# Performance work log

Measured on AMD Instinct MI355X. Metric: run time of the kernel, lower is better.

## Reference

```python
import jax, jax.numpy as jnp
import numpy as np
import math

B, N, CZ, CH, H, NRBF = 1, 256, 128, 32, 4, 39
INF = 1e8
DMIN, DMAX = 3.25 / 10.0, 50.75 / 10.0
EPS = 1e-5


def _ln(x, g, b):
    mu = x.mean(-1, keepdims=True)
    var = ((x - mu) ** 2).mean(-1, keepdims=True)
    return (x - mu) / jnp.sqrt(var + EPS) * g + b


def _rbf(D):
    mu = jnp.linspace(DMIN, DMAX, NRBF)
    sigma = (DMAX - DMIN) / NRBF
    return jnp.exp(-(((D[..., None] - mu) / sigma) ** 2))  # [B,N,N,NRBF]


def _tri_attn(z, mask_bias, edge_bias, ln_g, ln_b, wq, wk, wv, wg, wo, starting):
    # z: [B,I,J,CZ]; mask_bias: [B,I,1,1,J]; edge_bias: [B,1,H,I,J]
    z = _ln(z, ln_g, ln_b)
    if not starting:
        z = jnp.swapaxes(z, -2, -3)
        mask_bias = jnp.swapaxes(mask_bias, -4, -1)
        edge_bias = jnp.swapaxes(edge_bias, -1, -2)
    sh = z.shape[:-1] + (H, CH)
    q = (z @ wq).reshape(sh)  # [B,I,Q,H,c]
    k = (z @ wk).reshape(sh)
    v = (z @ wv).reshape(sh)
    logits = jnp.einsum('biqhc,bikhc->bihqk', q, k) / math.sqrt(CH)
    logits = logits + mask_bias + edge_bias  # [B,I,H,Q,K]
    a = jax.nn.softmax(logits, axis=-1)
    o = jnp.einsum('bihqk,bikhc->biqhc', a, v)  # [B,I,Q,H,c]
    g = jax.nn.sigmoid((z @ wg).reshape(sh))
    o = (o * g).reshape(z.shape[:-1] + (H * CH,)) @ wo  # [B,I,Q,CZ]
    if not starting:
        o = jnp.swapaxes(o, -2, -3)
    return o


def setup_inputs() -> dict:
    key = jax.random.key(0)
    ks = iter(jax.random.split(key, 32))
    def w(shape, fan_in):
        return jax.random.normal(next(ks), shape, dtype=jnp.float32) / math.sqrt(fan_in)
    inp = {
        'edge_embed': jax.random.normal(next(ks), (B, N, N, CZ), dtype=jnp.float32),
        'coords': jax.random.normal(next(ks), (B, N, 3), dtype=jnp.float32),
        'edge_mask': jnp.ones((B, N, N), dtype=jnp.float32),
        'emb_rbf_w1': w((NRBF, CH), NRBF),
        'emb_rbf_ln_g': jnp.ones((CH,), jnp.float32),
        'emb_rbf_ln_b': jnp.zeros((CH,), jnp.float32),
        'emb_rbf_w2': w((CH, H), CH),
        'ln3_g': jnp.ones((CZ,), jnp.float32),
        'ln3_b': jnp.zeros((CZ,), jnp.float32),
        'emb_third_w': w((CZ, H), CZ),
    }
    for p in ('s', 'e'):
        inp[p + '_ln_g'] = jnp.ones((CZ,), jnp.float32)
        inp[p + '_ln_b'] = jnp.zeros((CZ,), jnp.float32)
        inp[p + '_wq'] = w((CZ, H * CH), CZ)
        inp[p + '_wk'] = w((CZ, H * CH), CZ)
        inp[p + '_wv'] = w((CZ, H * CH), CZ)
        inp[p + '_wg'] = w((CZ, H * CH), CZ)
        inp[p + '_wo'] = w((H * CH, CZ), H * CH)
    return inp


def reference(edge_embed, coords, edge_mask,
              emb_rbf_w1, emb_rbf_ln_g, emb_rbf_ln_b, emb_rbf_w2,
              ln3_g, ln3_b, emb_third_w,
              s_ln_g, s_ln_b, s_wq, s_wk, s_wv, s_wg, s_wo,
              e_ln_g, e_ln_b, e_wq, e_wk, e_wv, e_wg, e_wo):
    # pairwise distances [B,N,N]
    diff = coords[:, :, None, :] - coords[:, None, :, :]
    dist = jnp.sqrt(jnp.sum(diff * diff, axis=-1) + 1e-12)
    h = _rbf(dist) @ emb_rbf_w1
    h = _ln(h, emb_rbf_ln_g, emb_rbf_ln_b)
    dist_bias = h @ emb_rbf_w2  # [B,N,N,H]
    mask_bias = (edge_mask[..., :, None, None, :] - 1.0) * INF  # [B,N,1,1,N]
    third = _ln(edge_embed, ln3_g, ln3_b) @ emb_third_w  # [B,N,N,H]
    edge_bias = (dist_bias + third)[:, None]  # [B,1,N,N,H]
    edge_bias = jnp.moveaxis(edge_bias, -1, -3)  # permute_final_dims (2,0,1) -> [B,1,H,N,N]
    z = edge_embed
    z = z + _tri_attn(z, mask_bias, edge_bias, s_ln_g, s_ln_b, s_wq, s_wk, s_wv, s_wg, s_wo, True)
    z = z + _tri_attn(z, mask_bias, edge_bias, e_ln_g, e_ln_b, e_wq, e_wk, e_wv, e_wg, e_wo, False)
    return z
```

## Files before the change

kernel.cpp:

```cpp
#include <hip/hip_runtime.h>

typedef unsigned short u16;
typedef unsigned int u32;
typedef __attribute__((ext_vector_type(4))) short short4v;
typedef __attribute__((ext_vector_type(8))) short short8;
typedef __attribute__((ext_vector_type(4))) float f32x4;
typedef __attribute__((ext_vector_type(4))) u32 u32x4;

__device__ __forceinline__ float bf2f(u16 u){ u32 x = ((u32)u)<<16; float f; __builtin_memcpy(&f,&x,4); return f; }
__device__ __forceinline__ u16 f2bf(float f){ u32 u; __builtin_memcpy(&u,&f,4); u32 r = (u + 0x7fffu + ((u>>16)&1u))>>16; return (u16)r; }

__device__ __forceinline__ float wsum64(float v){
  #pragma unroll
  for (int m=32;m>=1;m>>=1) v += __shfl_xor(v,m,64);
  return v;
}
__device__ __forceinline__ float wsum32(float v){
  #pragma unroll
  for (int m=16;m>=1;m>>=1) v += __shfl_xor(v,m,64);
  return v;
}

struct WPtrs { const float* s[10]; u16* d[10]; };

__global__ __launch_bounds__(256) void kconv_all(WPtrs wp){
  int mid = blockIdx.x>>6;
  int t = (blockIdx.x&63)*256 + threadIdx.x;
  int n = t>>7, k = t&127;
  wp.d[mid][n*128+k] = f2bf(wp.s[mid][k*128+n]);
}

__global__ __launch_bounds__(256) void kprep(
    const float* __restrict__ ee, const float* __restrict__ coords,
    const float* __restrict__ w1, const float* __restrict__ rg, const float* __restrict__ rbta,
    const float* __restrict__ w2, const float* __restrict__ g3, const float* __restrict__ b3,
    const float* __restrict__ w3, const float* __restrict__ gs, const float* __restrict__ bs,
    const float* __restrict__ mask,
    u16* __restrict__ zln, u16* __restrict__ ebx0, u16* __restrict__ ebxT,
    float* __restrict__ maskE)
{
  int wid = (blockIdx.x*256 + threadIdx.x)>>6;
  int lane = threadIdx.x & 63;
  int i = wid>>8, j = wid&255;
  float dx = coords[i*3+0]-coords[j*3+0];
  float dy = coords[i*3+1]-coords[j*3+1];
  float dz = coords[i*3+2]-coords[j*3+2];
  float dist = sqrtf(dx*dx+dy*dy+dz*dz+1e-12f);
  float rbv = 0.f;
  if (lane<39){ float t = (dist-(0.325f+0.125f*(float)lane))*8.210526315789474f; rbv = __expf(-t*t); }
  int c = lane&31;
  float hacc = 0.f;
  #pragma unroll
  for (int r=0;r<39;r++){ float rv = __shfl(rbv,r,64); hacc = fmaf(rv, w1[r*32+c], hacc); }
  float mu = wsum32(hacc)*(1.f/32.f);
  float vr = wsum32(hacc*hacc)*(1.f/32.f) - mu*mu;
  float hn = (hacc-mu)*rsqrtf(vr+1e-5f)*rg[c]+rbta[c];
  float db0 = wsum32(hn*w2[c*4+0]);
  float db1 = wsum32(hn*w2[c*4+1]);
  float db2 = wsum32(hn*w2[c*4+2]);
  float db3 = wsum32(hn*w2[c*4+3]);
  int c0 = lane*2, c1 = lane*2+1;
  float x0 = ee[(size_t)wid*128+c0], x1 = ee[(size_t)wid*128+c1];
  float m2 = wsum64(x0+x1)*(1.f/128.f);
  float v2 = wsum64(x0*x0+x1*x1)*(1.f/128.f)-m2*m2;
  float rinv = rsqrtf(v2+1e-5f);
  float n0 = (x0-m2)*rinv, n1 = (x1-m2)*rinv;
  u32 pk = (u32)f2bf(n0*gs[c0]+bs[c0]) | ((u32)f2bf(n1*gs[c1]+bs[c1])<<16);
  ((u32*)zln)[(size_t)wid*64+lane] = pk;
  float t0 = n0*g3[c0]+b3[c0], t1 = n1*g3[c1]+b3[c1];
  float th0 = wsum64(t0*w3[c0*4+0]+t1*w3[c1*4+0]);
  float th1 = wsum64(t0*w3[c0*4+1]+t1*w3[c1*4+1]);
  float th2 = wsum64(t0*w3[c0*4+2]+t1*w3[c1*4+2]);
  float th3 = wsum64(t0*w3[c0*4+3]+t1*w3[c1*4+3]);
  if (lane<4){
    float v = (lane==0)?(db0+th0):(lane==1)?(db1+th1):(lane==2)?(db2+th2):(db3+th3);
    u16 ev = f2bf(__expf(v));
    int h = lane;
    ebx0[(((size_t)(h*16+(i>>4))*16+(j>>4))*256) + ((j&15)+((i>>2)&3)*16)*4 + (i&3)] = ev;
    ebxT[(((size_t)(h*16+(j>>4))*16+(i>>4))*256) + ((i&15)+((j>>2)&3)*16)*4 + (j&3)] = ev;
  }
  if (lane==4) maskE[(size_t)j*256+i] = mask[(size_t)wid];
}

#define QB_OFF 0
#define KB_OFF 9216
#define VB_OFF 18432
#define PB_OFF 27008
__global__ __launch_bounds__(512,1) void kfused(const u16* __restrict__ zln, const u16* __restrict__ wT,
                                                const u16* __restrict__ ebx, const float* __restrict__ maskp,
                                                u16* __restrict__ og){
  __shared__ u16 S[61312];
  const int i = blockIdx.x, tid = threadIdx.x;
  const int w = tid>>6, lane = tid&63, r16 = lane&15, gq = lane>>4;
  #pragma unroll
  for (int r=0;r<8;r++){
    int chunk = tid + 512*r;
    int row = chunk>>4, off = (chunk&15)*8;
    *(u32x4*)&S[row*136+off] = *(const u32x4*)&zln[((size_t)i*256+row)*128+off];
  }
  __syncthreads();
  short8 a[2][4];
  #pragma unroll
  for (int mt=0;mt<2;mt++)
    #pragma unroll
    for (int ks=0;ks<4;ks++)
      a[mt][ks] = *(const short8*)&S[(w*32+mt*16+r16)*136 + ks*32 + gq*8];
  float pm[16];
  const float* mrow = maskp + (size_t)i*256;
  #pragma unroll
  for (int kt=0;kt<16;kt++)
    pm[kt] = (mrow[kt*16+r16] > 0.999f) ? 1.f : 0.f;

  u16* Pw = &S[PB_OFF + w*4288];

  for (int h=0; h<4; h++){
    f32x4 accQ[2][2], accK[2][2], accV[2][2], accG[2][2];
    #pragma unroll
    for (int mt=0;mt<2;mt++)
      #pragma unroll
      for (int nt=0;nt<2;nt++){
        accQ[mt][nt]=(f32x4){0,0,0,0}; accK[mt][nt]=(f32x4){0,0,0,0};
        accV[mt][nt]=(f32x4){0,0,0,0}; accG[mt][nt]=(f32x4){0,0,0,0};
      }
    #pragma unroll
    for (int nt=0;nt<2;nt++)
      #pragma unroll
      for (int ks=0;ks<4;ks++){
        short8 b0 = *(const short8*)&wT[(size_t)(0*128 + h*32 + nt*16 + r16)*128 + ks*32 + gq*8];
        short8 b1 = *(const short8*)&wT[(size_t)(1*128 + h*32 + nt*16 + r16)*128 + ks*32 + gq*8];
        short8 b2 = *(const short8*)&wT[(size_t)(2*128 + h*32 + nt*16 + r16)*128 + ks*32 + gq*8];
        short8 b3 = *(const short8*)&wT[(size_t)(3*128 + h*32 + nt*16 + r16)*128 + ks*32 + gq*8];
        #pragma unroll
        for (int mt=0;mt<2;mt++){
          accQ[mt][nt] = __builtin_amdgcn_mfma_f32_16x16x32_bf16(a[mt][ks], b0, accQ[mt][nt], 0,0,0);
          accK[mt][nt] = __builtin_amdgcn_mfma_f32_16x16x32_bf16(a[mt][ks], b1, accK[mt][nt], 0,0,0);
          accV[mt][nt] = __builtin_amdgcn_mfma_f32_16x16x32_bf16(a[mt][ks], b2, accV[mt][nt], 0,0,0);
          accG[mt][nt] = __builtin_amdgcn_mfma_f32_16x16x32_bf16(a[mt][ks], b3, accG[mt][nt], 0,0,0);
        }
      }
    __syncthreads();
    #pragma unroll
    for (int mt=0;mt<2;mt++)
      #pragma unroll
      for (int nt=0;nt<2;nt++)
        #pragma unroll
        for (int reg=0;reg<4;reg++){
          int row = w*32+mt*16+gq*4+reg, col = nt*16+r16;
          S[QB_OFF + row*36 + col] = f2bf(accQ[mt][nt][reg]);
          S[KB_OFF + row*36 + col] = f2bf(accK[mt][nt][reg]);
          S[VB_OFF + col*268 + row] = f2bf(accV[mt][nt][reg]);
        }
    __syncthreads();
    const u16* ebt = ebx + (size_t)h*16*16*256;
    #pragma unroll
    for (int qs=0; qs<2; qs++){
      const int qt = w*2+qs;
      short8 aq;
      *(short4v*)&aq      = *(const short4v*)&S[QB_OFF + (qt*16+r16)*36 + gq*8];
      *((short4v*)&aq+1)  = *(const short4v*)&S[QB_OFF + (qt*16+r16)*36 + gq*8 + 4];
      float sums[4] = {0.f,0.f,0.f,0.f};
      #pragma unroll
      for (int half=0;half<2;half++){
        f32x4 s[8];
        #pragma unroll
        for (int kt2=0;kt2<8;kt2++){
          int kt = half*8+kt2;
          short8 bk;
          *(short4v*)&bk     = *(const short4v*)&S[KB_OFF + (kt*16+r16)*36 + gq*8];
          *((short4v*)&bk+1) = *(const short4v*)&S[KB_OFF + (kt*16+r16)*36 + gq*8 + 4];
          f32x4 z = {0.f,0.f,0.f,0.f};
          s[kt2] = __builtin_amdgcn_mfma_f32_16x16x32_bf16(aq, bk, z, 0,0,0);
        }
        #pragma unroll
        for (int kt2=0;kt2<8;kt2++){
          int kt = half*8+kt2;
          int kk = kt*16 + r16;
          uint2 er = *(const uint2*)&ebt[((size_t)(qt*16+kt)*64 + lane)*4];
          u16 e4[4]; __builtin_memcpy(e4, &er, 8);
          #pragma unroll
          for (int reg=0;reg<4;reg++){
            float e = __expf(s[kt2][reg]*0.17677669529663687f) * bf2f(e4[reg]) * pm[kt];
            sums[reg] += e;
            Pw[(gq*4+reg)*268 + kk] = f2bf(e);
          }
        }
      }
      #pragma unroll
      for (int reg=0;reg<4;reg++){
        #pragma unroll
        for (int mm=1;mm<=8;mm<<=1) sums[reg] += __shfl_xor(sums[reg],mm,64);
        sums[reg] = 1.f/sums[reg];
      }
      f32x4 o[2]; o[0]=(f32x4){0.f,0.f,0.f,0.f}; o[1]=(f32x4){0.f,0.f,0.f,0.f};
      #pragma unroll
      for (int ks=0;ks<8;ks++){
        short8 ap;
        *(short4v*)&ap     = *(const short4v*)&Pw[r16*268 + ks*32 + gq*8];
        *((short4v*)&ap+1) = *(const short4v*)&Pw[r16*268 + ks*32 + gq*8 + 4];
        #pragma unroll
        for (int ct=0;ct<2;ct++){
          short8 bv;
          *(short4v*)&bv     = *(const short4v*)&S[VB_OFF + (ct*16+r16)*268 + ks*32 + gq*8];
          *((short4v*)&bv+1) = *(const short4v*)&S[VB_OFF + (ct*16+r16)*268 + ks*32 + gq*8 + 4];
          o[ct] = __builtin_amdgcn_mfma_f32_16x16x32_bf16(ap, bv, o[ct], 0,0,0);
        }
      }
      #pragma unroll
      for (int ct=0;ct<2;ct++)
        #pragma unroll
        for (int reg=0;reg<4;reg++){
          float gv = 1.f/(1.f+__expf(-accG[qs][ct][reg]));
          Pw[(gq*4+reg)*40 + ct*16+r16] = f2bf(o[ct][reg]*sums[reg]*gv);
        }
      u32x4 odat = *(const u32x4*)&Pw[(lane>>2)*40 + (lane&3)*8];
      *(u32x4*)&og[((size_t)i*256 + qt*16 + (lane>>2))*128 + h*32 + (lane&3)*8] = odat;
    }
  }
}

__global__ __launch_bounds__(256) void kproj(const u16* __restrict__ og, const u16* __restrict__ woT,
                                             const float* __restrict__ resid, float* __restrict__ out,
                                             u16* __restrict__ zln, const float* __restrict__ eg,
                                             const float* __restrict__ eb, const int epass){
  const int m0 = blockIdx.x*128;
  __shared__ u16 A[128*136];
  const int tid = threadIdx.x;
  #pragma unroll
  for (int r=0;r<8;r++){
    int chunk = tid + 256*r;
    int row = chunk>>4, off = (chunk&15)*8;
    *(u32x4*)&A[row*136+off] = *(const u32x4*)&og[(size_t)(m0+row)*128+off];
  }
  __syncthreads();
  const int w = tid>>6, lane = tid&63, r16 = lane&15, gq = lane>>4;
  short8 a[2][4];
  #pragma unroll
  for (int mt=0;mt<2;mt++)
    #pragma unroll
    for (int ks=0;ks<4;ks++)
      a[mt][ks] = *(const short8*)&A[(w*32+mt*16+r16)*136 + ks*32 + gq*8];
  f32x4 acc[2][8];
  #pragma unroll
  for (int mt=0;mt<2;mt++)
    #pragma unroll
    for (int nt=0;nt<8;nt++)
      acc[mt][nt] = (f32x4){0.f,0.f,0.f,0.f};
  #pragma unroll
  for (int nt=0;nt<8;nt++){
    short8 bq[4];
    #pragma unroll
    for (int ks=0;ks<4;ks++)
      bq[ks] = *(const short8*)&woT[(size_t)(nt*16+r16)*128 + ks*32 + gq*8];
    #pragma unroll
    for (int mt=0;mt<2;mt++)
      #pragma unroll
      for (int ks=0;ks<4;ks++)
        acc[mt][nt] = __builtin_amdgcn_mfma_f32_16x16x32_bf16(a[mt][ks], bq[ks], acc[mt][nt], 0,0,0);
  }
  if (epass){
    #pragma unroll
    for (int mt=0;mt<2;mt++){
      int mbase = m0+w*32+mt*16+gq*4;
      #pragma unroll
      for (int nt=0;nt<8;nt++){
        int n = nt*16+r16;
        #pragma unroll
        for (int reg=0;reg<4;reg++){
          int m = mbase+reg;
          size_t idx = ((size_t)((m&255)*256+(m>>8)))*128+(size_t)n;
          out[idx] = resid[idx] + acc[mt][nt][reg];
        }
      }
    }
  } else {
    __syncthreads();
    #pragma unroll
    for (int mt=0;mt<2;mt++){
      int mbase = m0+w*32+mt*16+gq*4;
      #pragma unroll
      for (int reg=0;reg<4;reg++){
        int m = mbase+reg;
        float s1 = 0.f, s2 = 0.f;
        #pragma unroll
        for (int nt=0;nt<8;nt++){
          int n = nt*16+r16;
          size_t idx = (size_t)m*128+(size_t)n;
          float v = resid[idx] + acc[mt][nt][reg];
          out[idx] = v;
          acc[mt][nt][reg] = v;
          s1 += v; s2 += v*v;
        }
        #pragma unroll
        for (int mm=1;mm<=8;mm<<=1){ s1 += __shfl_xor(s1,mm,64); s2 += __shfl_xor(s2,mm,64); }
        float mean = s1*(1.f/128.f);
        float rinv = rsqrtf(s2*(1.f/128.f)-mean*mean+1e-5f);
        #pragma unroll
        for (int nt=0;nt<8;nt++){
          int n = nt*16+r16;
          A[(m-m0)*136 + n] = f2bf((acc[mt][nt][reg]-mean)*rinv*eg[n]+eb[n]);
        }
      }
    }
    __syncthreads();
    const int i = m0>>8, jb = m0&255;
    #pragma unroll
    for (int it=0; it<8; it++){
      int chunk = it*256+tid;
      int rl = chunk>>4, c8 = (chunk&15)*8;
      u32x4 vdat = *(const u32x4*)&A[rl*136 + c8];
      *(u32x4*)&zln[((size_t)(jb+rl)*256 + i)*128 + c8] = vdat;
    }
  }
}

extern "C" void kernel_launch(void* const* d_in, const int* in_sizes, int n_in,
                              void* d_out, int out_size, void* d_ws, size_t ws_size,
                              hipStream_t stream) {
  const float* ee     = (const float*)d_in[0];
  const float* coords = (const float*)d_in[1];
  const float* mask   = (const float*)d_in[2];
  const float* w1     = (const float*)d_in[3];
  const float* rg     = (const float*)d_in[4];
  const float* rbta   = (const float*)d_in[5];
  const float* w2     = (const float*)d_in[6];
  const float* g3     = (const float*)d_in[7];
  const float* b3     = (const float*)d_in[8];
  const float* w3     = (const float*)d_in[9];
  const float* sln_g  = (const float*)d_in[10];
  const float* sln_b  = (const float*)d_in[11];
  const float* eln_g  = (const float*)d_in[17];
  const float* eln_b  = (const float*)d_in[18];
  float* out = (float*)d_out;
  char* ws = (char*)d_ws;

  u16*   wT_s  = (u16*)(ws + 0);
  u16*   wT_e  = (u16*)(ws + 131072);
  u16*   woT_s = (u16*)(ws + 262144);
  u16*   woT_e = (u16*)(ws + 294912);
  u16*   ebx0  = (u16*)(ws + 327680);
  u16*   ebxT  = (u16*)(ws + 851968);
  float* maskE = (float*)(ws + 1376256);
  u16*   zln   = (u16*)(ws + 1638400);
  u16*   og    = (u16*)(ws + 18415616);

  WPtrs wp;
  for (int s=0;s<4;s++){ wp.s[s] = (const float*)d_in[12+s]; wp.d[s] = wT_s + s*128*128; }
  wp.s[4] = (const float*)d_in[16]; wp.d[4] = woT_s;
  for (int s=0;s<4;s++){ wp.s[5+s] = (const float*)d_in[19+s]; wp.d[5+s] = wT_e + s*128*128; }
  wp.s[9] = (const float*)d_in[23]; wp.d[9] = woT_e;
  kconv_all<<<640,256,0,stream>>>(wp);

  kprep<<<16384,256,0,stream>>>(ee, coords, w1, rg, rbta, w2, g3, b3, w3, sln_g, sln_b,
                                mask, zln, ebx0, ebxT, maskE);

  kfused<<<256,512,0,stream>>>(zln, wT_s, ebx0, mask, og);
  kproj<<<512,256,0,stream>>>(og, woT_s, ee, out, zln, eln_g, eln_b, 0);

  kfused<<<256,512,0,stream>>>(zln, wT_e, ebxT, maskE, og);
  kproj<<<512,256,0,stream>>>(og, woT_e, out, out, nullptr, nullptr, nullptr, 1);
}
```

Measured before the change: 438.6 us.

## Split fused attention across heads per block and swizzle LDS layouts for MFMA

The fused triangle-attention kernel now launches one 256-thread block per (row, head) pair instead of one 512-thread block looping over all four heads, with two blocks per CU. Each wave loads its z rows straight from global memory, and Q/K/V are stored in MFMA-fragment-ordered LDS layouts so each operand is a single 16-byte read. The P buffer uses an XOR swizzle to avoid bank conflicts. The RBF prep also computes the exponentials per lane instead of broadcasting them through shuffles. The aim is more parallelism and less LDS traffic, at the cost of reloading z once per head and recomputing the RBF exponentials in every lane.

```diff
diff --git a/kernel.cpp b/kernel.cpp
--- a/kernel.cpp
+++ b/kernel.cpp
@@ -2,7 +2,6 @@
 
 typedef unsigned short u16;
 typedef unsigned int u32;
-typedef __attribute__((ext_vector_type(4))) short short4v;
 typedef __attribute__((ext_vector_type(8))) short short8;
 typedef __attribute__((ext_vector_type(4))) float f32x4;
 typedef __attribute__((ext_vector_type(4))) u32 u32x4;
@@ -46,12 +45,18 @@
   float dy = coords[i*3+1]-coords[j*3+1];
   float dz = coords[i*3+2]-coords[j*3+2];
   float dist = sqrtf(dx*dx+dy*dy+dz*dz+1e-12f);
-  float rbv = 0.f;
-  if (lane<39){ float t = (dist-(0.325f+0.125f*(float)lane))*8.210526315789474f; rbv = __expf(-t*t); }
   int c = lane&31;
-  float hacc = 0.f;
-  #pragma unroll
-  for (int r=0;r<39;r++){ float rv = __shfl(rbv,r,64); hacc = fmaf(rv, w1[r*32+c], hacc); }
+  float hacc0 = 0.f, hacc1 = 0.f;
+  #pragma unroll
+  for (int r=0;r<39;r+=2){
+    float t0 = (dist-(0.325f+0.125f*(float)r))*8.210526315789474f;
+    hacc0 = fmaf(__expf(-t0*t0), w1[r*32+c], hacc0);
+    if (r+1<39){
+      float t1 = (dist-(0.325f+0.125f*(float)(r+1)))*8.210526315789474f;
+      hacc1 = fmaf(__expf(-t1*t1), w1[(r+1)*32+c], hacc1);
+    }
+  }
+  float hacc = hacc0 + hacc1;
   float mu = wsum32(hacc)*(1.f/32.f);
   float vr = wsum32(hacc*hacc)*(1.f/32.f) - mu*mu;
   float hn = (hacc-mu)*rsqrtf(vr+1e-5f)*rg[c]+rbta[c];
@@ -82,139 +87,121 @@
   if (lane==4) maskE[(size_t)j*256+i] = mask[(size_t)wid];
 }
 
-#define QB_OFF 0
-#define KB_OFF 9216
-#define VB_OFF 18432
-#define PB_OFF 27008
-__global__ __launch_bounds__(512,1) void kfused(const u16* __restrict__ zln, const u16* __restrict__ wT,
+#define QS 0
+#define KS 8192
+#define VS 16384
+#define PS 24576
+__global__ __launch_bounds__(256,2) void kfused(const u16* __restrict__ zln, const u16* __restrict__ wT,
                                                 const u16* __restrict__ ebx, const float* __restrict__ maskp,
                                                 u16* __restrict__ og){
-  __shared__ u16 S[61312];
-  const int i = blockIdx.x, tid = threadIdx.x;
+  __shared__ u16 S[40960];
+  const int i = blockIdx.x, h = blockIdx.y, tid = threadIdx.x;
   const int w = tid>>6, lane = tid&63, r16 = lane&15, gq = lane>>4;
-  #pragma unroll
-  for (int r=0;r<8;r++){
-    int chunk = tid + 512*r;
-    int row = chunk>>4, off = (chunk&15)*8;
-    *(u32x4*)&S[row*136+off] = *(const u32x4*)&zln[((size_t)i*256+row)*128+off];
-  }
-  __syncthreads();
-  short8 a[2][4];
-  #pragma unroll
-  for (int mt=0;mt<2;mt++)
+  short8 a[4][4];
+  const u16* zb = zln + (size_t)i*32768;
+  #pragma unroll
+  for (int mt=0;mt<4;mt++)
     #pragma unroll
     for (int ks=0;ks<4;ks++)
-      a[mt][ks] = *(const short8*)&S[(w*32+mt*16+r16)*136 + ks*32 + gq*8];
+      a[mt][ks] = *(const short8*)&zb[(w*64 + mt*16 + r16)*128 + ks*32 + gq*8];
   float pm[16];
   const float* mrow = maskp + (size_t)i*256;
   #pragma unroll
   for (int kt=0;kt<16;kt++)
     pm[kt] = (mrow[kt*16+r16] > 0.999f) ? 1.f : 0.f;
 
-  u16* Pw = &S[PB_OFF + w*4288];
-
-  for (int h=0; h<4; h++){
-    f32x4 accQ[2][2], accK[2][2], accV[2][2], accG[2][2];
-    #pragma unroll
-    for (int mt=0;mt<2;mt++)
-      #pragma unroll
-      for (int nt=0;nt<2;nt++){
-        accQ[mt][nt]=(f32x4){0,0,0,0}; accK[mt][nt]=(f32x4){0,0,0,0};
-        accV[mt][nt]=(f32x4){0,0,0,0}; accG[mt][nt]=(f32x4){0,0,0,0};
-      }
+  f32x4 accG[4][2];
+  #pragma unroll
+  for (int sel=0; sel<4; sel++){
+    f32x4 acc[4][2];
+    #pragma unroll
+    for (int mt=0;mt<4;mt++){ acc[mt][0]=(f32x4){0,0,0,0}; acc[mt][1]=(f32x4){0,0,0,0}; }
     #pragma unroll
     for (int nt=0;nt<2;nt++)
       #pragma unroll
       for (int ks=0;ks<4;ks++){
-        short8 b0 = *(const short8*)&wT[(size_t)(0*128 + h*32 + nt*16 + r16)*128 + ks*32 + gq*8];
-        short8 b1 = *(const short8*)&wT[(size_t)(1*128 + h*32 + nt*16 + r16)*128 + ks*32 + gq*8];
-        short8 b2 = *(const short8*)&wT[(size_t)(2*128 + h*32 + nt*16 + r16)*128 + ks*32 + gq*8];
-        short8 b3 = *(const short8*)&wT[(size_t)(3*128 + h*32 + nt*16 + r16)*128 + ks*32 + gq*8];
-        #pragma unroll
-        for (int mt=0;mt<2;mt++){
-          accQ[mt][nt] = __builtin_amdgcn_mfma_f32_16x16x32_bf16(a[mt][ks], b0, accQ[mt][nt], 0,0,0);
-          accK[mt][nt] = __builtin_amdgcn_mfma_f32_16x16x32_bf16(a[mt][ks], b1, accK[mt][nt], 0,0,0);
-          accV[mt][nt] = __builtin_amdgcn_mfma_f32_16x16x32_bf16(a[mt][ks], b2, accV[mt][nt], 0,0,0);
-          accG[mt][nt] = __builtin_amdgcn_mfma_f32_16x16x32_bf16(a[mt][ks], b3, accG[mt][nt], 0,0,0);
-        }
-      }
-    __syncthreads();
-    #pragma unroll
-    for (int mt=0;mt<2;mt++)
-      #pragma unroll
-      for (int nt=0;nt<2;nt++)
-        #pragma unroll
-        for (int reg=0;reg<4;reg++){
-          int row = w*32+mt*16+gq*4+reg, col = nt*16+r16;
-          S[QB_OFF + row*36 + col] = f2bf(accQ[mt][nt][reg]);
-          S[KB_OFF + row*36 + col] = f2bf(accK[mt][nt][reg]);
-          S[VB_OFF + col*268 + row] = f2bf(accV[mt][nt][reg]);
-        }
-    __syncthreads();
-    const u16* ebt = ebx + (size_t)h*16*16*256;
-    #pragma unroll
-    for (int qs=0; qs<2; qs++){
-      const int qt = w*2+qs;
-      short8 aq;
-      *(short4v*)&aq      = *(const short4v*)&S[QB_OFF + (qt*16+r16)*36 + gq*8];
-      *((short4v*)&aq+1)  = *(const short4v*)&S[QB_OFF + (qt*16+r16)*36 + gq*8 + 4];
-      float sums[4] = {0.f,0.f,0.f,0.f};
-      #pragma unroll
-      for (int half=0;half<2;half++){
-        f32x4 s[8];
-        #pragma unroll
-        for (int kt2=0;kt2<8;kt2++){
-          int kt = half*8+kt2;
-          short8 bk;
-          *(short4v*)&bk     = *(const short4v*)&S[KB_OFF + (kt*16+r16)*36 + gq*8];
-          *((short4v*)&bk+1) = *(const short4v*)&S[KB_OFF + (kt*16+r16)*36 + gq*8 + 4];
-          f32x4 z = {0.f,0.f,0.f,0.f};
-          s[kt2] = __builtin_amdgcn_mfma_f32_16x16x32_bf16(aq, bk, z, 0,0,0);
-        }
-        #pragma unroll
-        for (int kt2=0;kt2<8;kt2++){
-          int kt = half*8+kt2;
-          int kk = kt*16 + r16;
-          uint2 er = *(const uint2*)&ebt[((size_t)(qt*16+kt)*64 + lane)*4];
-          u16 e4[4]; __builtin_memcpy(e4, &er, 8);
+        short8 bq = *(const short8*)&wT[((size_t)sel*128 + h*32 + nt*16 + r16)*128 + ks*32 + gq*8];
+        #pragma unroll
+        for (int mt=0;mt<4;mt++)
+          acc[mt][nt] = __builtin_amdgcn_mfma_f32_16x16x32_bf16(a[mt][ks], bq, acc[mt][nt], 0,0,0);
+      }
+    if (sel==3){
+      #pragma unroll
+      for (int mt=0;mt<4;mt++){ accG[mt][0]=acc[mt][0]; accG[mt][1]=acc[mt][1]; }
+    } else {
+      #pragma unroll
+      for (int mt=0;mt<4;mt++)
+        #pragma unroll
+        for (int nt=0;nt<2;nt++)
           #pragma unroll
           for (int reg=0;reg<4;reg++){
-            float e = __expf(s[kt2][reg]*0.17677669529663687f) * bf2f(e4[reg]) * pm[kt];
-            sums[reg] += e;
-            Pw[(gq*4+reg)*268 + kk] = f2bf(e);
+            int row = w*64 + mt*16 + gq*4 + reg;
+            int c   = nt*16 + r16;
+            u16 v = f2bf(acc[mt][nt][reg]);
+            if (sel==0)      S[QS + (row>>4)*512 + (row&15)*8 + (c>>3)*128 + (c&7)] = v;
+            else if (sel==1) S[KS + (row>>4)*512 + (row&15)*8 + (c>>3)*128 + (c&7)] = v;
+            else             S[VS + ((row>>5)*2 + nt)*512 + ((c&15) + ((row&31)>>3)*16)*8 + (row&7)] = v;
           }
+    }
+  }
+  __syncthreads();
+
+  const u16* ebt = ebx + (size_t)h*16*16*256;
+  char* Pb = (char*)&S[PS + w*4096];
+  for (int qs=0; qs<4; qs++){
+    const int qt = w*4+qs;
+    short8 aq = *(const short8*)&S[QS + qt*512 + lane*8];
+    float sums[4] = {0.f,0.f,0.f,0.f};
+    #pragma unroll
+    for (int half=0;half<2;half++){
+      f32x4 s[8];
+      #pragma unroll
+      for (int kt2=0;kt2<8;kt2++){
+        short8 bk = *(const short8*)&S[KS + (half*8+kt2)*512 + lane*8];
+        f32x4 z = {0.f,0.f,0.f,0.f};
+        s[kt2] = __builtin_amdgcn_mfma_f32_16x16x32_bf16(aq, bk, z, 0,0,0);
+      }
+      #pragma unroll
+      for (int kt2=0;kt2<8;kt2++){
+        int kt = half*8+kt2;
+        int kk = kt*16 + r16;
+        uint2 er = *(const uint2*)&ebt[((size_t)(qt*16+kt)*64 + lane)*4];
+        u16 e4[4]; __builtin_memcpy(e4, &er, 8);
+        #pragma unroll
+        for (int reg=0;reg<4;reg++){
+          float e = __expf(s[kt2][reg]*0.17677669529663687f) * bf2f(e4[reg]) * pm[kt];
+          sums[reg] += e;
+          int row = gq*4+reg;
+          *(u16*)(Pb + ((row*512 + kk*2) ^ ((row&7)<<4))) = f2bf(e);
         }
       }
+    }
+    #pragma unroll
+    for (int reg=0;reg<4;reg++){
+      #pragma unroll
+      for (int mm=1;mm<=8;mm<<=1) sums[reg] += __shfl_xor(sums[reg],mm,64);
+      sums[reg] = 1.f/sums[reg];
+    }
+    f32x4 o[2]; o[0]=(f32x4){0.f,0.f,0.f,0.f}; o[1]=(f32x4){0.f,0.f,0.f,0.f};
+    #pragma unroll
+    for (int ks=0;ks<8;ks++){
+      short8 ap = *(const short8*)(Pb + ((r16*512 + ks*64 + gq*16) ^ ((r16&7)<<4)));
+      #pragma unroll
+      for (int ct=0;ct<2;ct++){
+        short8 bv = *(const short8*)&S[VS + (ks*2+ct)*512 + lane*8];
+        o[ct] = __builtin_amdgcn_mfma_f32_16x16x32_bf16(ap, bv, o[ct], 0,0,0);
+      }
+    }
+    u16* Ob = (u16*)Pb;
+    #pragma unroll
+    for (int ct=0;ct<2;ct++)
       #pragma unroll
       for (int reg=0;reg<4;reg++){
-        #pragma unroll
-        for (int mm=1;mm<=8;mm<<=1) sums[reg] += __shfl_xor(sums[reg],mm,64);
-        sums[reg] = 1.f/sums[reg];
-      }
-      f32x4 o[2]; o[0]=(f32x4){0.f,0.f,0.f,0.f}; o[1]=(f32x4){0.f,0.f,0.f,0.f};
-      #pragma unroll
-      for (int ks=0;ks<8;ks++){
-        short8 ap;
-        *(short4v*)&ap     = *(const short4v*)&Pw[r16*268 + ks*32 + gq*8];
-        *((short4v*)&ap+1) = *(const short4v*)&Pw[r16*268 + ks*32 + gq*8 + 4];
-        #pragma unroll
-        for (int ct=0;ct<2;ct++){
-          short8 bv;
-          *(short4v*)&bv     = *(const short4v*)&S[VB_OFF + (ct*16+r16)*268 + ks*32 + gq*8];
-          *((short4v*)&bv+1) = *(const short4v*)&S[VB_OFF + (ct*16+r16)*268 + ks*32 + gq*8 + 4];
-          o[ct] = __builtin_amdgcn_mfma_f32_16x16x32_bf16(ap, bv, o[ct], 0,0,0);
-        }
-      }
-      #pragma unroll
-      for (int ct=0;ct<2;ct++)
-        #pragma unroll
-        for (int reg=0;reg<4;reg++){
-          float gv = 1.f/(1.f+__expf(-accG[qs][ct][reg]));
-          Pw[(gq*4+reg)*40 + ct*16+r16] = f2bf(o[ct][reg]*sums[reg]*gv);
-        }
-      u32x4 odat = *(const u32x4*)&Pw[(lane>>2)*40 + (lane&3)*8];
-      *(u32x4*)&og[((size_t)i*256 + qt*16 + (lane>>2))*128 + h*32 + (lane&3)*8] = odat;
-    }
+        float gv = 1.f/(1.f+__expf(-accG[qs][ct][reg]));
+        Ob[(gq*4+reg)*40 + ct*16+r16] = f2bf(o[ct][reg]*sums[reg]*gv);
+      }
+    u32x4 odat = *(const u32x4*)&Ob[(lane>>2)*40 + (lane&3)*8];
+    *(u32x4*)&og[((size_t)i*256 + qt*16 + (lane>>2))*128 + h*32 + (lane&3)*8] = odat;
   }
 }
 
@@ -353,9 +340,9 @@
   kprep<<<16384,256,0,stream>>>(ee, coords, w1, rg, rbta, w2, g3, b3, w3, sln_g, sln_b,
                                 mask, zln, ebx0, ebxT, maskE);
 
-  kfused<<<256,512,0,stream>>>(zln, wT_s, ebx0, mask, og);
+  kfused<<<dim3(256,4),256,0,stream>>>(zln, wT_s, ebx0, mask, og);
   kproj<<<512,256,0,stream>>>(og, woT_s, ee, out, zln, eln_g, eln_b, 0);
 
-  kfused<<<256,512,0,stream>>>(zln, wT_e, ebxT, maskE, og);
+  kfused<<<dim3(256,4),256,0,stream>>>(zln, wT_e, ebxT, maskE, og);
   kproj<<<512,256,0,stream>>>(og, woT_e, out, out, nullptr, nullptr, nullptr, 1);
 }
```

After: 392.7 us. 10.4% less time.
